# Performance work log

Hardware: AMD Instinct MI355X
Metric: run time of the kernel (lower is better)

Reference implementation:

```python
import jax, jax.numpy as jnp
import numpy as np

H = 8
D = 64
EPS = 1e-5
TEMP = 1.0


def _ln(x, w, b):
    m = jnp.mean(x, axis=-1, keepdims=True)
    v = jnp.var(x, axis=-1, keepdims=True)
    return (x - m) * jax.lax.rsqrt(v + EPS) * w + b


def setup_inputs() -> dict:
    key = jax.random.key(0)
    ks = jax.random.split(key, 8)
    B, T, C = 4, 1024, 512
    x = jax.random.normal(ks[0], (B, T, C), dtype=jnp.float32)
    pair = jax.random.normal(ks[1], (B, T, T, H), dtype=jnp.float32)
    mask = jax.random.randint(ks[2], (B, T, T), 0, 2).astype(bool)
    s = 0.02
    return {
        "x": x,
        "pair": pair,
        "mask": mask,
        "norm_w": jnp.ones((C,), jnp.float32),
        "norm_b": jnp.zeros((C,), jnp.float32),
        "qkv_w": jax.random.normal(ks[3], (3 * C, C), jnp.float32) * s,
        "qkv_b": jnp.zeros((3 * C,), jnp.float32),
        "qln_w": jnp.ones((C,), jnp.float32),
        "qln_b": jnp.zeros((C,), jnp.float32),
        "kln_w": jnp.ones((C,), jnp.float32),
        "kln_b": jnp.zeros((C,), jnp.float32),
        "proj_w": jax.random.normal(ks[4], (C, C), jnp.float32) * s,
        "proj_b": jnp.zeros((C,), jnp.float32),
    }


def reference(x, pair, mask, norm_w, norm_b, qkv_w, qkv_b, qln_w, qln_b,
              kln_w, kln_b, proj_w, proj_b):
    B, T, C = x.shape
    # pre-norm
    xn = _ln(x, norm_w, norm_b)
    qkv = xn @ qkv_w.T + qkv_b  # [B,T,3C]
    q, k, v = jnp.split(qkv, 3, axis=-1)
    q = _ln(q, qln_w, qln_b)
    k = _ln(k, kln_w, kln_b)
    # [B,T,C] -> [B,H,T,D]
    to_heads = lambda t: t.reshape(B, T, H, D).transpose(0, 2, 1, 3)
    q, k, v = to_heads(q), to_heads(k), to_heads(v)
    scale = (D ** -0.5) / TEMP
    sim = jnp.einsum("bhid,bhjd->bhij", q, k) * scale
    sim = sim + pair.transpose(0, 3, 1, 2)  # additive pair bias [B,H,T,T]
    neg = jnp.finfo(sim.dtype).min
    sim = jnp.where(mask[:, None, :, :], sim, sim + neg)
    attn = jax.nn.softmax(sim, axis=-1)
    out = jnp.einsum("bhij,bhjd->bhid", attn, v)
    out = out.transpose(0, 2, 1, 3).reshape(B, T, C)
    return out @ proj_w.T + proj_b
```

## Files before the change

kernel.cpp:

```cpp
#include <hip/hip_runtime.h>
#include <math.h>

#define B_  4
#define T_  1024
#define C_  512
#define H_  8
#define D_  64
#define N3_ 1536
#define BT_ 4096

constexpr float kEps = 1e-5f;
constexpr float kNeg = -3.4028234663852886e38f;

typedef __attribute__((ext_vector_type(8))) short bf16x8;
typedef __attribute__((ext_vector_type(4))) float f32x4;

__device__ __forceinline__ short f2bf(float f) {
  union { float f; unsigned u; } v; v.f = f;
  unsigned r = v.u + 0x7FFFu + ((v.u >> 16) & 1u);
  return (short)(r >> 16);
}

__global__ __launch_bounds__(64) void mask_detect_kernel(
    const unsigned int* __restrict__ m, int* __restrict__ flag) {
  int lane = threadIdx.x;
  int any_big = 0;
#pragma unroll
  for (int p = 0; p < 16; ++p) {
    unsigned int v = m[lane + p * 64];
    any_big |= (v > 1u);
  }
  unsigned long long b = __ballot(any_big);
  if (lane == 0) flag[0] = (b != 0ull) ? 1 : 0;
}

__global__ __launch_bounds__(256) void mask_convert_kernel(
    const void* __restrict__ mraw, const int* __restrict__ flag,
    uchar4* __restrict__ out) {
  int idx = blockIdx.x * 256 + threadIdx.x;
  uchar4 v;
  if (flag[0]) {
    v = ((const uchar4*)mraw)[idx];
    v.x = v.x ? 1 : 0; v.y = v.y ? 1 : 0; v.z = v.z ? 1 : 0; v.w = v.w ? 1 : 0;
  } else {
    int4 w = ((const int4*)mraw)[idx];
    v = make_uchar4(w.x != 0, w.y != 0, w.z != 0, w.w != 0);
  }
  out[idx] = v;
}

__global__ __launch_bounds__(256) void wcvt_kernel(
    const float* __restrict__ in, short* __restrict__ out) {
  int i = (blockIdx.x * 256 + threadIdx.x) * 4;
  float4 v = *(const float4*)&in[i];
  short4 o;
  o.x = f2bf(v.x); o.y = f2bf(v.y); o.z = f2bf(v.z); o.w = f2bf(v.w);
  *(short4*)&out[i] = o;
}

__global__ __launch_bounds__(128) void ln_x_kernel(
    const float* __restrict__ x, const float* __restrict__ w,
    const float* __restrict__ b, short* __restrict__ xn) {
  int row = blockIdx.x;
  int tid = threadIdx.x;
  const float* xr = x + (size_t)row * C_;
  float4 v = *(const float4*)&xr[tid * 4];
  float s  = v.x + v.y + v.z + v.w;
  float ss = v.x * v.x + v.y * v.y + v.z * v.z + v.w * v.w;
#pragma unroll
  for (int o = 32; o > 0; o >>= 1) {
    s  += __shfl_down(s, o);
    ss += __shfl_down(ss, o);
  }
  __shared__ float sh[4];
  int wid = tid >> 6, lane = tid & 63;
  if (lane == 0) { sh[wid] = s; sh[2 + wid] = ss; }
  __syncthreads();
  float m   = (sh[0] + sh[1]) * (1.0f / C_);
  float var = (sh[2] + sh[3]) * (1.0f / C_) - m * m;
  float inv = rsqrtf(var + kEps);
  float4 wv = *(const float4*)&w[tid * 4];
  float4 bv = *(const float4*)&b[tid * 4];
  short4 o4;
  o4.x = f2bf((v.x - m) * inv * wv.x + bv.x);
  o4.y = f2bf((v.y - m) * inv * wv.y + bv.y);
  o4.z = f2bf((v.z - m) * inv * wv.z + bv.z);
  o4.w = f2bf((v.w - m) * inv * wv.w + bv.w);
  *(short4*)&xn[(size_t)row * C_ + tid * 4] = o4;
}

__global__ __launch_bounds__(256) void gemm_bf16_kernel(
    const short* __restrict__ A, const short* __restrict__ W,
    const float* __restrict__ bias, float* __restrict__ Cmat,
    int M, int N, int K) {
  __shared__ short As[128 * 72];
  __shared__ short Bs[64 * 72];
  int tid = threadIdx.x;
  int lane = tid & 63, wave = tid >> 6;
  int wm = wave >> 1, wn = wave & 1;
  int col = lane & 15, quad = lane >> 4;
  int m0 = blockIdx.y * 128, n0 = blockIdx.x * 64;

  f32x4 acc[4][2];
#pragma unroll
  for (int mi = 0; mi < 4; ++mi)
#pragma unroll
    for (int ni = 0; ni < 2; ++ni) acc[mi][ni] = {0.f, 0.f, 0.f, 0.f};

  for (int k0 = 0; k0 < K; k0 += 64) {
    __syncthreads();
#pragma unroll
    for (int p = 0; p < 4; ++p) {
      int c = tid + p * 256;
      int row = c >> 3, kc = (c & 7) * 8;
      *(int4*)&As[row * 72 + kc] =
          *(const int4*)&A[(size_t)(m0 + row) * K + k0 + kc];
    }
#pragma unroll
    for (int p = 0; p < 2; ++p) {
      int c = tid + p * 256;
      int row = c >> 3, kc = (c & 7) * 8;
      *(int4*)&Bs[row * 72 + kc] =
          *(const int4*)&W[(size_t)(n0 + row) * K + k0 + kc];
    }
    __syncthreads();
#pragma unroll
    for (int s = 0; s < 2; ++s) {
      bf16x8 af[4], bf[2];
#pragma unroll
      for (int mi = 0; mi < 4; ++mi)
        af[mi] = *(const bf16x8*)&As[(64 * wm + 16 * mi + col) * 72 + s * 32 + quad * 8];
#pragma unroll
      for (int ni = 0; ni < 2; ++ni)
        bf[ni] = *(const bf16x8*)&Bs[(32 * wn + 16 * ni + col) * 72 + s * 32 + quad * 8];
#pragma unroll
      for (int mi = 0; mi < 4; ++mi)
#pragma unroll
        for (int ni = 0; ni < 2; ++ni)
          acc[mi][ni] = __builtin_amdgcn_mfma_f32_16x16x32_bf16(
              af[mi], bf[ni], acc[mi][ni], 0, 0, 0);
    }
  }
#pragma unroll
  for (int ni = 0; ni < 2; ++ni) {
    int n = n0 + 32 * wn + 16 * ni + col;
    float bv = bias[n];
#pragma unroll
    for (int mi = 0; mi < 4; ++mi) {
#pragma unroll
      for (int r = 0; r < 4; ++r) {
        int m = m0 + 64 * wm + 16 * mi + quad * 4 + r;
        Cmat[(size_t)m * N + n] = acc[mi][ni][r] + bv;
      }
    }
  }
}

__global__ __launch_bounds__(128) void qkv_ln_split_kernel(
    const float* __restrict__ qkv,
    const float* __restrict__ qw, const float* __restrict__ qb,
    const float* __restrict__ kw, const float* __restrict__ kb,
    short* __restrict__ qh, short* __restrict__ kh, short* __restrict__ vh) {
  int row = blockIdx.x;
  int b = row >> 10, t = row & 1023;
  int tid = threadIdx.x;
  const float* base = qkv + (size_t)row * N3_;
  int c4 = tid * 4;
  float4 qv = *(const float4*)&base[c4];
  float4 kv = *(const float4*)&base[C_ + c4];
  float4 vv = *(const float4*)&base[2 * C_ + c4];
  float sq  = qv.x + qv.y + qv.z + qv.w;
  float sqq = qv.x * qv.x + qv.y * qv.y + qv.z * qv.z + qv.w * qv.w;
  float sk  = kv.x + kv.y + kv.z + kv.w;
  float skk = kv.x * kv.x + kv.y * kv.y + kv.z * kv.z + kv.w * kv.w;
#pragma unroll
  for (int o = 32; o > 0; o >>= 1) {
    sq  += __shfl_down(sq, o);
    sqq += __shfl_down(sqq, o);
    sk  += __shfl_down(sk, o);
    skk += __shfl_down(skk, o);
  }
  __shared__ float sh[8];
  int wid = tid >> 6, lane = tid & 63;
  if (lane == 0) { sh[wid] = sq; sh[2 + wid] = sqq; sh[4 + wid] = sk; sh[6 + wid] = skk; }
  __syncthreads();
  float qm   = (sh[0] + sh[1]) * (1.0f / C_);
  float qvar = (sh[2] + sh[3]) * (1.0f / C_) - qm * qm;
  float km   = (sh[4] + sh[5]) * (1.0f / C_);
  float kvar = (sh[6] + sh[7]) * (1.0f / C_) - km * km;
  float qi = rsqrtf(qvar + kEps);
  float ki = rsqrtf(kvar + kEps);
  float4 qwv = *(const float4*)&qw[c4];
  float4 qbv = *(const float4*)&qb[c4];
  float4 kwv = *(const float4*)&kw[c4];
  float4 kbv = *(const float4*)&kb[c4];
  int h = tid >> 4;
  int d = (tid & 15) * 4;
  size_t dst = ((size_t)(b * H_ + h) * T_ + t) * D_ + d;
  short4 qo, ko, vo;
  qo.x = f2bf((qv.x - qm) * qi * qwv.x + qbv.x);
  qo.y = f2bf((qv.y - qm) * qi * qwv.y + qbv.y);
  qo.z = f2bf((qv.z - qm) * qi * qwv.z + qbv.z);
  qo.w = f2bf((qv.w - qm) * qi * qwv.w + qbv.w);
  ko.x = f2bf((kv.x - km) * ki * kwv.x + kbv.x);
  ko.y = f2bf((kv.y - km) * ki * kwv.y + kbv.y);
  ko.z = f2bf((kv.z - km) * ki * kwv.z + kbv.z);
  ko.w = f2bf((kv.w - km) * ki * kwv.w + kbv.w);
  vo.x = f2bf(vv.x); vo.y = f2bf(vv.y); vo.z = f2bf(vv.z); vo.w = f2bf(vv.w);
  *(short4*)&qh[dst] = qo;
  *(short4*)&kh[dst] = ko;
  *(short4*)&vh[dst] = vo;
}

__global__ __launch_bounds__(256) void attn_kernel(
    const short* __restrict__ qh, const short* __restrict__ kh,
    const short* __restrict__ vh, const float* __restrict__ pair,
    const unsigned char* __restrict__ mask, short* __restrict__ ao) {
  __shared__ short Ks[64 * 72];
  __shared__ short Vt[64 * 72];
  __shared__ short Ps[64 * 72];
  int tid = threadIdx.x;
  int lane = tid & 63, w = tid >> 6;
  int col = lane & 15, quad = lane >> 4;
  int bh = blockIdx.y;
  int b = bh >> 3, h = bh & 7;
  int i0 = blockIdx.x * 64;
  const short* Qg = qh + (size_t)bh * T_ * D_;
  const short* Kg = kh + (size_t)bh * T_ * D_;
  const short* Vg = vh + (size_t)bh * T_ * D_;

  bf16x8 qf[2];
#pragma unroll
  for (int s = 0; s < 2; ++s)
    qf[s] = *(const bf16x8*)&Qg[(size_t)(i0 + 16 * w + col) * D_ + s * 32 + quad * 8];

  float mrun[4], lrun[4];
  f32x4 oacc[4];
#pragma unroll
  for (int r = 0; r < 4; ++r) { mrun[r] = -INFINITY; lrun[r] = 0.f; }
#pragma unroll
  for (int dt = 0; dt < 4; ++dt) oacc[dt] = {0.f, 0.f, 0.f, 0.f};

  for (int j0 = 0; j0 < T_; j0 += 64) {
    __syncthreads();
#pragma unroll
    for (int p = 0; p < 2; ++p) {
      int c = tid + p * 256;
      int row = c >> 3, dc = (c & 7) * 8;
      *(int4*)&Ks[row * 72 + dc] =
          *(const int4*)&Kg[(size_t)(j0 + row) * D_ + dc];
    }
    {
      int j = tid & 63, d0 = (tid >> 6) * 16;
#pragma unroll
      for (int p = 0; p < 2; ++p) {
        short tmp[8];
        *(int4*)tmp = *(const int4*)&Vg[(size_t)(j0 + j) * D_ + d0 + p * 8];
#pragma unroll
        for (int q = 0; q < 8; ++q) Vt[(d0 + p * 8 + q) * 72 + j] = tmp[q];
      }
    }
    __syncthreads();

    f32x4 sacc[4];
#pragma unroll
    for (int jt = 0; jt < 4; ++jt) sacc[jt] = {0.f, 0.f, 0.f, 0.f};
#pragma unroll
    for (int s = 0; s < 2; ++s) {
#pragma unroll
      for (int jt = 0; jt < 4; ++jt) {
        bf16x8 kf = *(const bf16x8*)&Ks[(16 * jt + col) * 72 + s * 32 + quad * 8];
        sacc[jt] = __builtin_amdgcn_mfma_f32_16x16x32_bf16(qf[s], kf, sacc[jt], 0, 0, 0);
      }
    }

#pragma unroll
    for (int r = 0; r < 4; ++r) {
      int gi = i0 + 16 * w + quad * 4 + r;
      const float* prow = pair + (size_t)(b * T_ + gi) * (T_ * H_) + h;
      const unsigned char* mrow = mask + (size_t)(b * T_ + gi) * T_;
      float sv[4];
      float rm = -INFINITY;
#pragma unroll
      for (int jt = 0; jt < 4; ++jt) {
        int j = j0 + 16 * jt + col;
        float s = fmaf(sacc[jt][r], 0.125f, prow[(size_t)j * H_]);
        if (!mrow[j]) s += kNeg;
        sv[jt] = s;
        rm = fmaxf(rm, s);
      }
#pragma unroll
      for (int o = 8; o > 0; o >>= 1) rm = fmaxf(rm, __shfl_xor(rm, o));
      float mnew  = fmaxf(mrun[r], rm);
      float alpha = __expf(mrun[r] - mnew);
      float psum = 0.f;
#pragma unroll
      for (int jt = 0; jt < 4; ++jt) {
        float p = __expf(sv[jt] - mnew);
        psum += p;
        Ps[(16 * w + quad * 4 + r) * 72 + 16 * jt + col] = f2bf(p);
      }
#pragma unroll
      for (int o = 8; o > 0; o >>= 1) psum += __shfl_xor(psum, o);
      lrun[r] = lrun[r] * alpha + psum;
      mrun[r] = mnew;
#pragma unroll
      for (int dt = 0; dt < 4; ++dt) oacc[dt][r] *= alpha;
    }
    __syncthreads();

#pragma unroll
    for (int s = 0; s < 2; ++s) {
      bf16x8 pf = *(const bf16x8*)&Ps[(16 * w + col) * 72 + s * 32 + quad * 8];
#pragma unroll
      for (int dt = 0; dt < 4; ++dt) {
        bf16x8 vf = *(const bf16x8*)&Vt[(16 * dt + col) * 72 + s * 32 + quad * 8];
        oacc[dt] = __builtin_amdgcn_mfma_f32_16x16x32_bf16(pf, vf, oacc[dt], 0, 0, 0);
      }
    }
  }

#pragma unroll
  for (int r = 0; r < 4; ++r) {
    int gi = i0 + 16 * w + quad * 4 + r;
    float inv = 1.0f / lrun[r];
    size_t base = (size_t)(b * T_ + gi) * C_ + h * D_;
#pragma unroll
    for (int dt = 0; dt < 4; ++dt)
      ao[base + 16 * dt + col] = f2bf(oacc[dt][r] * inv);
  }
}

extern "C" void kernel_launch(void* const* d_in, const int* in_sizes, int n_in,
                              void* d_out, int out_size, void* d_ws, size_t ws_size,
                              hipStream_t stream) {
  const float* x      = (const float*)d_in[0];
  const float* pair   = (const float*)d_in[1];
  const void*  maskraw = d_in[2];
  const float* norm_w = (const float*)d_in[3];
  const float* norm_b = (const float*)d_in[4];
  const float* qkv_w  = (const float*)d_in[5];
  const float* qkv_b  = (const float*)d_in[6];
  const float* qln_w  = (const float*)d_in[7];
  const float* qln_b  = (const float*)d_in[8];
  const float* kln_w  = (const float*)d_in[9];
  const float* kln_b  = (const float*)d_in[10];
  const float* proj_w = (const float*)d_in[11];
  const float* proj_b = (const float*)d_in[12];
  float* out = (float*)d_out;

  short* xn = (short*)d_out;
  short* qh = (short*)d_out + (size_t)BT_ * C_;

  float* qkv = (float*)d_ws;
  short* ao  = (short*)d_ws;
  short* sw  = (short*)d_ws;
  short* wq  = sw + (size_t)12 * 1024 * 1024;
  short* wp  = wq + (size_t)N3_ * C_;
  short* kh  = sw + (size_t)13 * 1024 * 1024;
  short* vh  = sw + (size_t)15 * 1024 * 1024;
  unsigned char* maskc = (unsigned char*)d_ws + (size_t)34 * 1024 * 1024;
  int* flag = (int*)((unsigned char*)d_ws + (size_t)38 * 1024 * 1024);

  mask_detect_kernel<<<1, 64, 0, stream>>>((const unsigned int*)maskraw, flag);
  mask_convert_kernel<<<(B_ * T_ * T_) / 1024, 256, 0, stream>>>(
      maskraw, flag, (uchar4*)maskc);
  wcvt_kernel<<<(N3_ * C_) / 1024, 256, 0, stream>>>(qkv_w, wq);
  wcvt_kernel<<<(C_ * C_) / 1024, 256, 0, stream>>>(proj_w, wp);
  ln_x_kernel<<<BT_, 128, 0, stream>>>(x, norm_w, norm_b, xn);
  gemm_bf16_kernel<<<dim3(N3_ / 64, BT_ / 128), 256, 0, stream>>>(
      xn, wq, qkv_b, qkv, BT_, N3_, C_);
  qkv_ln_split_kernel<<<BT_, 128, 0, stream>>>(
      qkv, qln_w, qln_b, kln_w, kln_b, qh, kh, vh);
  attn_kernel<<<dim3(T_ / 64, B_ * H_), 256, 0, stream>>>(
      qh, kh, vh, pair, maskc, ao);
  gemm_bf16_kernel<<<dim3(C_ / 64, BT_ / 128), 256, 0, stream>>>(
      ao, wp, proj_b, out, BT_, C_, C_);
}
```

Before: 345.2 us.

## Pre-transpose pair bias with mask folded into bf16 per-head layout

Adds a prep kernel that reads the [B,T,T,H] pair tensor once, converts it to bf16, folds the mask in as a large negative value, and writes it transposed to [B,H,T,T]. A new attention kernel then reads contiguous bf16 bias rows instead of strided fp32 pair loads plus a separate mask byte. The 1/sqrt(D) scale is folded into q during the LN/split kernel. This adds an extra 64MB write/read pass and bf16 rounding of the bias, and depends on the workspace being at least 80MB, otherwise the old path runs.

```diff
diff --git a/kernel.cpp b/kernel.cpp
--- a/kernel.cpp
+++ b/kernel.cpp
@@ -11,6 +11,7 @@
 
 constexpr float kEps = 1e-5f;
 constexpr float kNeg = -3.4028234663852886e38f;
+constexpr float kMaskNeg = -1e38f;
 
 typedef __attribute__((ext_vector_type(8))) short bf16x8;
 typedef __attribute__((ext_vector_type(4))) float f32x4;
@@ -19,6 +20,11 @@
   union { float f; unsigned u; } v; v.f = f;
   unsigned r = v.u + 0x7FFFu + ((v.u >> 16) & 1u);
   return (short)(r >> 16);
+}
+__device__ __forceinline__ float bf2f(unsigned short b) {
+  union { unsigned u; float f; } v;
+  v.u = ((unsigned)b) << 16;
+  return v.f;
 }
 
 __global__ __launch_bounds__(64) void mask_detect_kernel(
@@ -47,6 +53,46 @@
     v = make_uchar4(w.x != 0, w.y != 0, w.z != 0, w.w != 0);
   }
   out[idx] = v;
+}
+
+__global__ __launch_bounds__(256) void pair_prep_kernel(
+    const float* __restrict__ pair, const void* __restrict__ mraw,
+    const int* __restrict__ flag, short* __restrict__ biast) {
+  __shared__ short P[8][1024 + 8];
+  int bi = blockIdx.x;
+  int b = bi >> 10, i = bi & 1023;
+  int tid = threadIdx.x;
+  const float* src = pair + (size_t)bi * (T_ * H_);
+#pragma unroll
+  for (int p = 0; p < 8; ++p) {
+    int c = tid + p * 256;
+    int j = c >> 1, hh = (c & 1) * 4;
+    float4 v = *(const float4*)&src[c * 4];
+    P[hh + 0][j] = f2bf(v.x);
+    P[hh + 1][j] = f2bf(v.y);
+    P[hh + 2][j] = f2bf(v.z);
+    P[hh + 3][j] = f2bf(v.w);
+  }
+  bool mk[4];
+  if (flag[0]) {
+    uchar4 mv = ((const uchar4*)mraw)[bi * 256 + tid];
+    mk[0] = mv.x; mk[1] = mv.y; mk[2] = mv.z; mk[3] = mv.w;
+  } else {
+    int4 mv = ((const int4*)mraw)[bi * 256 + tid];
+    mk[0] = mv.x != 0; mk[1] = mv.y != 0; mk[2] = mv.z != 0; mk[3] = mv.w != 0;
+  }
+  __syncthreads();
+  const short negb = f2bf(kMaskNeg);
+  int j = tid * 4;
+#pragma unroll
+  for (int h = 0; h < 8; ++h) {
+    short4 o;
+    o.x = mk[0] ? P[h][j + 0] : negb;
+    o.y = mk[1] ? P[h][j + 1] : negb;
+    o.z = mk[2] ? P[h][j + 2] : negb;
+    o.w = mk[3] ? P[h][j + 3] : negb;
+    *(short4*)&biast[((size_t)(b * 8 + h) * T_ + i) * T_ + j] = o;
+  }
 }
 
 __global__ __launch_bounds__(256) void wcvt_kernel(
@@ -198,10 +244,10 @@
   int d = (tid & 15) * 4;
   size_t dst = ((size_t)(b * H_ + h) * T_ + t) * D_ + d;
   short4 qo, ko, vo;
-  qo.x = f2bf((qv.x - qm) * qi * qwv.x + qbv.x);
-  qo.y = f2bf((qv.y - qm) * qi * qwv.y + qbv.y);
-  qo.z = f2bf((qv.z - qm) * qi * qwv.z + qbv.z);
-  qo.w = f2bf((qv.w - qm) * qi * qwv.w + qbv.w);
+  qo.x = f2bf(((qv.x - qm) * qi * qwv.x + qbv.x) * 0.125f);
+  qo.y = f2bf(((qv.y - qm) * qi * qwv.y + qbv.y) * 0.125f);
+  qo.z = f2bf(((qv.z - qm) * qi * qwv.z + qbv.z) * 0.125f);
+  qo.w = f2bf(((qv.w - qm) * qi * qwv.w + qbv.w) * 0.125f);
   ko.x = f2bf((kv.x - km) * ki * kwv.x + kbv.x);
   ko.y = f2bf((kv.y - km) * ki * kwv.y + kbv.y);
   ko.z = f2bf((kv.z - km) * ki * kwv.z + kbv.z);
@@ -210,6 +256,123 @@
   *(short4*)&qh[dst] = qo;
   *(short4*)&kh[dst] = ko;
   *(short4*)&vh[dst] = vo;
+}
+
+__global__ __launch_bounds__(256) void attn_bias_kernel(
+    const short* __restrict__ qh, const short* __restrict__ kh,
+    const short* __restrict__ vh, const short* __restrict__ biast,
+    short* __restrict__ ao) {
+  __shared__ short Ks[64 * 72];
+  __shared__ short Vt[64 * 72];
+  __shared__ short Ps[64 * 72];
+  int tid = threadIdx.x;
+  int lane = tid & 63, w = tid >> 6;
+  int col = lane & 15, quad = lane >> 4;
+  int bh = blockIdx.y;
+  int b = bh >> 3;
+  int i0 = blockIdx.x * 64;
+  const short* Qg = qh + (size_t)bh * T_ * D_;
+  const short* Kg = kh + (size_t)bh * T_ * D_;
+  const short* Vg = vh + (size_t)bh * T_ * D_;
+  const unsigned short* Bp = (const unsigned short*)biast + (size_t)bh * T_ * T_;
+
+  bf16x8 qf[2];
+#pragma unroll
+  for (int s = 0; s < 2; ++s)
+    qf[s] = *(const bf16x8*)&Qg[(size_t)(i0 + 16 * w + col) * D_ + s * 32 + quad * 8];
+
+  float mrun[4], lrun[4];
+  f32x4 oacc[4];
+#pragma unroll
+  for (int r = 0; r < 4; ++r) { mrun[r] = -INFINITY; lrun[r] = 0.f; }
+#pragma unroll
+  for (int dt = 0; dt < 4; ++dt) oacc[dt] = {0.f, 0.f, 0.f, 0.f};
+
+  for (int j0 = 0; j0 < T_; j0 += 64) {
+    __syncthreads();
+#pragma unroll
+    for (int p = 0; p < 2; ++p) {
+      int c = tid + p * 256;
+      int row = c >> 3, dc = (c & 7) * 8;
+      *(int4*)&Ks[row * 72 + dc] =
+          *(const int4*)&Kg[(size_t)(j0 + row) * D_ + dc];
+    }
+    {
+      int j = tid & 63, d0 = (tid >> 6) * 16;
+#pragma unroll
+      for (int p = 0; p < 2; ++p) {
+        short tmp[8];
+        *(int4*)tmp = *(const int4*)&Vg[(size_t)(j0 + j) * D_ + d0 + p * 8];
+#pragma unroll
+        for (int q = 0; q < 8; ++q) Vt[(d0 + p * 8 + q) * 72 + j] = tmp[q];
+      }
+    }
+    __syncthreads();
+
+    f32x4 sacc[4];
+#pragma unroll
+    for (int jt = 0; jt < 4; ++jt) sacc[jt] = {0.f, 0.f, 0.f, 0.f};
+#pragma unroll
+    for (int s = 0; s < 2; ++s) {
+#pragma unroll
+      for (int jt = 0; jt < 4; ++jt) {
+        bf16x8 kf = *(const bf16x8*)&Ks[(16 * jt + col) * 72 + s * 32 + quad * 8];
+        sacc[jt] = __builtin_amdgcn_mfma_f32_16x16x32_bf16(qf[s], kf, sacc[jt], 0, 0, 0);
+      }
+    }
+
+#pragma unroll
+    for (int r = 0; r < 4; ++r) {
+      int gi = i0 + 16 * w + quad * 4 + r;
+      const unsigned short* brow = Bp + (size_t)gi * T_ + j0;
+      float sv[4];
+      float rm = -INFINITY;
+#pragma unroll
+      for (int jt = 0; jt < 4; ++jt) {
+        float s = sacc[jt][r] + bf2f(brow[16 * jt + col]);
+        sv[jt] = s;
+        rm = fmaxf(rm, s);
+      }
+#pragma unroll
+      for (int o = 8; o > 0; o >>= 1) rm = fmaxf(rm, __shfl_xor(rm, o));
+      float mnew  = fmaxf(mrun[r], rm);
+      float alpha = __expf(mrun[r] - mnew);
+      float psum = 0.f;
+#pragma unroll
+      for (int jt = 0; jt < 4; ++jt) {
+        float p = __expf(sv[jt] - mnew);
+        psum += p;
+        Ps[(16 * w + quad * 4 + r) * 72 + 16 * jt + col] = f2bf(p);
+      }
+#pragma unroll
+      for (int o = 8; o > 0; o >>= 1) psum += __shfl_xor(psum, o);
+      lrun[r] = lrun[r] * alpha + psum;
+      mrun[r] = mnew;
+#pragma unroll
+      for (int dt = 0; dt < 4; ++dt) oacc[dt][r] *= alpha;
+    }
+    __syncthreads();
+
+#pragma unroll
+    for (int s = 0; s < 2; ++s) {
+      bf16x8 pf = *(const bf16x8*)&Ps[(16 * w + col) * 72 + s * 32 + quad * 8];
+#pragma unroll
+      for (int dt = 0; dt < 4; ++dt) {
+        bf16x8 vf = *(const bf16x8*)&Vt[(16 * dt + col) * 72 + s * 32 + quad * 8];
+        oacc[dt] = __builtin_amdgcn_mfma_f32_16x16x32_bf16(pf, vf, oacc[dt], 0, 0, 0);
+      }
+    }
+  }
+
+#pragma unroll
+  for (int r = 0; r < 4; ++r) {
+    int gi = i0 + 16 * w + quad * 4 + r;
+    float inv = 1.0f / lrun[r];
+    size_t base = (size_t)(b * T_ + gi) * C_ + (bh & 7) * D_;
+#pragma unroll
+    for (int dt = 0; dt < 4; ++dt)
+      ao[base + 16 * dt + col] = f2bf(oacc[dt][r] * inv);
+  }
 }
 
 __global__ __launch_bounds__(256) void attn_kernel(
@@ -284,7 +447,7 @@
 #pragma unroll
       for (int jt = 0; jt < 4; ++jt) {
         int j = j0 + 16 * jt + col;
-        float s = fmaf(sacc[jt][r], 0.125f, prow[(size_t)j * H_]);
+        float s = sacc[jt][r] + prow[(size_t)j * H_];
         if (!mrow[j]) s += kNeg;
         sv[jt] = s;
         rm = fmaxf(rm, s);
@@ -352,28 +515,57 @@
   short* xn = (short*)d_out;
   short* qh = (short*)d_out + (size_t)BT_ * C_;
 
-  float* qkv = (float*)d_ws;
-  short* ao  = (short*)d_ws;
-  short* sw  = (short*)d_ws;
-  short* wq  = sw + (size_t)12 * 1024 * 1024;
-  short* wp  = wq + (size_t)N3_ * C_;
-  short* kh  = sw + (size_t)13 * 1024 * 1024;
-  short* vh  = sw + (size_t)15 * 1024 * 1024;
-  unsigned char* maskc = (unsigned char*)d_ws + (size_t)34 * 1024 * 1024;
-  int* flag = (int*)((unsigned char*)d_ws + (size_t)38 * 1024 * 1024);
-
-  mask_detect_kernel<<<1, 64, 0, stream>>>((const unsigned int*)maskraw, flag);
-  mask_convert_kernel<<<(B_ * T_ * T_) / 1024, 256, 0, stream>>>(
-      maskraw, flag, (uchar4*)maskc);
-  wcvt_kernel<<<(N3_ * C_) / 1024, 256, 0, stream>>>(qkv_w, wq);
-  wcvt_kernel<<<(C_ * C_) / 1024, 256, 0, stream>>>(proj_w, wp);
-  ln_x_kernel<<<BT_, 128, 0, stream>>>(x, norm_w, norm_b, xn);
-  gemm_bf16_kernel<<<dim3(N3_ / 64, BT_ / 128), 256, 0, stream>>>(
-      xn, wq, qkv_b, qkv, BT_, N3_, C_);
-  qkv_ln_split_kernel<<<BT_, 128, 0, stream>>>(
-      qkv, qln_w, qln_b, kln_w, kln_b, qh, kh, vh);
-  attn_kernel<<<dim3(T_ / 64, B_ * H_), 256, 0, stream>>>(
-      qh, kh, vh, pair, maskc, ao);
-  gemm_bf16_kernel<<<dim3(C_ / 64, BT_ / 128), 256, 0, stream>>>(
-      ao, wp, proj_b, out, BT_, C_, C_);
-}
+  const size_t MB = 1024 * 1024;
+  bool big_ws = ws_size >= 80 * MB;
+
+  if (big_ws) {
+    char* base = (char*)d_ws;
+    short* biast = (short*)base;
+    float* qkv   = (float*)base;
+    short* ao    = (short*)(base + 64 * MB);
+    short* kh    = (short*)(base + 68 * MB);
+    short* vh    = (short*)(base + 72 * MB);
+    short* wq    = (short*)(base + 76 * MB);
+    short* wp    = (short*)(base + 77 * MB + 512 * 1024);
+    int*   flag  = (int*)(base + 78 * MB);
+
+    mask_detect_kernel<<<1, 64, 0, stream>>>((const unsigned int*)maskraw, flag);
+    wcvt_kernel<<<(N3_ * C_) / 1024, 256, 0, stream>>>(qkv_w, wq);
+    wcvt_kernel<<<(C_ * C_) / 1024, 256, 0, stream>>>(proj_w, wp);
+    ln_x_kernel<<<BT_, 128, 0, stream>>>(x, norm_w, norm_b, xn);
+    gemm_bf16_kernel<<<dim3(N3_ / 64, BT_ / 128), 256, 0, stream>>>(
+        xn, wq, qkv_b, qkv, BT_, N3_, C_);
+    qkv_ln_split_kernel<<<BT_, 128, 0, stream>>>(
+        qkv, qln_w, qln_b, kln_w, kln_b, qh, kh, vh);
+    pair_prep_kernel<<<B_ * T_, 256, 0, stream>>>(pair, maskraw, flag, biast);
+    attn_bias_kernel<<<dim3(T_ / 64, B_ * H_), 256, 0, stream>>>(
+        qh, kh, vh, biast, ao);
+    gemm_bf16_kernel<<<dim3(C_ / 64, BT_ / 128), 256, 0, stream>>>(
+        ao, wp, proj_b, out, BT_, C_, C_);
+  } else {
+    float* qkv = (float*)d_ws;
+    short* ao  = (short*)d_ws;
+    short* sw  = (short*)d_ws;
+    short* wq  = sw + (size_t)12 * 1024 * 1024;
+    short* wp  = wq + (size_t)N3_ * C_;
+    short* kh  = sw + (size_t)13 * 1024 * 1024;
+    short* vh  = sw + (size_t)15 * 1024 * 1024;
+    unsigned char* maskc = (unsigned char*)d_ws + (size_t)34 * MB;
+    int* flag = (int*)((unsigned char*)d_ws + (size_t)38 * MB);
+
+    mask_detect_kernel<<<1, 64, 0, stream>>>((const unsigned int*)maskraw, flag);
+    mask_convert_kernel<<<(B_ * T_ * T_) / 1024, 256, 0, stream>>>(
+        maskraw, flag, (uchar4*)maskc);
+    wcvt_kernel<<<(N3_ * C_) / 1024, 256, 0, stream>>>(qkv_w, wq);
+    wcvt_kernel<<<(C_ * C_) / 1024, 256, 0, stream>>>(proj_w, wp);
+    ln_x_kernel<<<BT_, 128, 0, stream>>>(x, norm_w, norm_b, xn);
+    gemm_bf16_kernel<<<dim3(N3_ / 64, BT_ / 128), 256, 0, stream>>>(
+        xn, wq, qkv_b, qkv, BT_, N3_, C_);
+    qkv_ln_split_kernel<<<BT_, 128, 0, stream>>>(
+        qkv, qln_w, qln_b, kln_w, kln_b, qh, kh, vh);
+    attn_kernel<<<dim3(T_ / 64, B_ * H_), 256, 0, stream>>>(
+        qh, kh, vh, pair, maskc, ao);
+    gemm_bf16_kernel<<<dim3(C_ / 64, BT_ / 128), 256, 0, stream>>>(
+        ao, wp, proj_b, out, BT_, C_, C_);
+  }
+}
```

New measurement: 324.4 us. 6.0% less time.
